# Performance work log

Hardware: AMD Instinct MI355X
Metric: run time of the kernel (lower is better)

## Reference

```python
import jax, jax.numpy as jnp
import numpy as np


def log_g(x):
    # faithful to torch: where(x>=0, log(relu(x)+0.5), 5 - softplus(-x))
    return jnp.where(x >= 0, jnp.log(jax.nn.relu(x) + 0.5), 5.0 - jax.nn.softplus(-x))


def setup_inputs() -> dict:
    key = jax.random.key(0)
    ks = jax.random.split(key, 6)
    B, T, D, H = 8, 4096, 1024, 1024
    s = 1.0 / np.sqrt(D)
    return {
        "x": jax.random.normal(ks[0], (B, T, D), jnp.float32),
        "h_0": jax.random.normal(ks[1], (B, 1, H), jnp.float32),
        "Wz_w": jax.random.normal(ks[2], (D, H), jnp.float32) * s,
        "Wz_b": jax.random.normal(ks[3], (H,), jnp.float32) * 0.1,
        "Wh_w": jax.random.normal(ks[4], (D, H), jnp.float32) * s,
        "Wh_b": jax.random.normal(ks[5], (H,), jnp.float32) * 0.1,
    }


def reference(x, h_0, Wz_w, Wz_b, Wh_w, Wh_b):
    # k = W_z(x)
    k = jnp.einsum('btd,dh->bth', x, Wz_w) + Wz_b
    log_z = -jax.nn.softplus(-k)          # log sigmoid(k)
    log_coeffs = -jax.nn.softplus(k)      # log(1 - sigmoid(k))
    log_h0 = log_g(h_0)                                            # [B,1,H]
    log_tilde_h = log_g(jnp.einsum('btd,dh->bth', x, Wh_w) + Wh_b)  # [B,T,H]
    log_values = jnp.concatenate([log_h0, log_z + log_tilde_h], axis=1)  # [B,T+1,H]
    # a_star = pad(cumsum(log_coeffs, dim=1), (0,0,1,0)) -> one zero row at t=0
    a_star = jnp.pad(jnp.cumsum(log_coeffs, axis=1), ((0, 0), (1, 0), (0, 0)))  # [B,T+1,H]
    log_h = a_star + jax.lax.cumlogsumexp(log_values - a_star, axis=1)
    return jnp.exp(log_h)[:, 1:]  # [B,T,H]
```

## Files before the change

### kernel.cpp

```cpp
#include <hip/hip_runtime.h>
#include <hip/hip_bf16.h>
#include <stdint.h>

#define B_   8
#define T_   4096
#define D_   1024
#define H_   1024
#define M_   (B_ * T_)
#define NC_  64
#define TC_  64


typedef __attribute__((ext_vector_type(4))) float f32x4;
typedef __attribute__((ext_vector_type(8))) short bfr8;
typedef _Float16 f16;
typedef __attribute__((ext_vector_type(2))) _Float16 f16x2;

__device__ __forceinline__ unsigned short f2bf(float f) {
  unsigned int u = __float_as_uint(f);
  u += 0x7fffu + ((u >> 16) & 1u);
  return (unsigned short)(u >> 16);
}
__device__ __forceinline__ float bf2f(unsigned short h) {
  return __uint_as_float(((unsigned int)h) << 16);
}

__device__ __forceinline__ void gload16(const void* g, void* l) {
  __builtin_amdgcn_global_load_lds((const __attribute__((address_space(1))) void*)g,
                                   (__attribute__((address_space(3))) void*)l,
                                   16, 0, 0);
}

__device__ __forceinline__ float g_of(float hv) {
  return (hv >= 0.f) ? (hv + 0.5f)
                     : 148.4131591025766f / (1.f + __expf(-hv));
}

__global__ void prep_w2(const float* __restrict__ Wz, const float* __restrict__ Wh,
                        unsigned short* __restrict__ wtp, float* __restrict__ whT,
                        unsigned int* __restrict__ fcnt)
{
  int kt = blockIdx.x;
  int nt = blockIdx.y;
  int m  = blockIdx.z;
  if (kt == 0 && nt == 0 && m == 0 && threadIdx.x == 0) *fcnt = 0u;
  __shared__ float tile[32][129];
  const float* W = m ? Wh : Wz;
  int n0 = nt * 128, k0 = kt * 32;
  int t = threadIdx.x;
  {
    int r = t >> 3, c0 = (t & 7) * 16;
    const float* src = &W[(size_t)(k0 + r) * 1024 + n0 + c0];
#pragma unroll
    for (int i = 0; i < 16; i++) tile[r][c0 + i] = src[i];
  }
  __syncthreads();
  unsigned short* out = wtp + ((size_t)(m * 8 + nt) * 32 + kt) * 8192;
  int n = t >> 1, hf = t & 1;
#pragma unroll
  for (int c4 = 0; c4 < 4; c4++) {
    int c = hf * 4 + c4;
    int s = c ^ (n & 7);
    unsigned int u[4];
#pragma unroll
    for (int q = 0; q < 4; q++) {
      unsigned short w2[2];
#pragma unroll
      for (int e2 = 0; e2 < 2; e2++) {
        int e = q * 2 + e2;
        float v = tile[(s & 3) * 8 + e][n];
        unsigned short hi = f2bf(v);
        w2[e2] = (s < 4) ? hi : f2bf(v - bf2f(hi));
      }
      u[q] = (unsigned int)w2[0] | ((unsigned int)w2[1] << 16);
    }
    *(uint4*)&out[(size_t)n * 64 + c * 8] = make_uint4(u[0], u[1], u[2], u[3]);
  }
  if (m == 1) {
#pragma unroll
    for (int i = 0; i < 16; i++)
      whT[(size_t)(n0 + n) * 1024 + k0 + hf * 16 + i] = tile[hf * 16 + i][n];
  }
}

__global__ __launch_bounds__(512, 2) void gemm_cv(
    const float* __restrict__ x,
    const unsigned short* __restrict__ wtp,
    const float* __restrict__ bz, const float* __restrict__ bhb,
    f16x2* __restrict__ cvbuf,
    unsigned int* __restrict__ fcnt, unsigned int* __restrict__ flist,
    unsigned int fcap)
{
  __shared__ __align__(16) unsigned short Ac[2][16384];
  __shared__ __align__(16) unsigned short Bz[2][8192];
  __shared__ __align__(16) unsigned short Bh[2][8192];
  int tid = threadIdx.x;
  int lane = tid & 63, wv = tid >> 6;
  int wm = wv >> 2, wn = wv & 3;
  int lrow = lane & 15, lq = lane >> 4;

  int bid = blockIdx.x;
  int cpx = gridDim.x >> 3;
  int swz = (bid & 7) * cpx + (bid >> 3);
  int nt = swz & 7;
  int mt = swz >> 3;
  int m0 = mt * 256, n0 = nt * 128;

  f32x4 accz[8][2], acch[8][2];
#pragma unroll
  for (int i = 0; i < 8; i++)
#pragma unroll
    for (int j = 0; j < 2; j++) {
      accz[i][j] = (f32x4){0.f, 0.f, 0.f, 0.f};
      acch[i][j] = (f32x4){0.f, 0.f, 0.f, 0.f};
    }

  int art = tid >> 1, half = tid & 1;
  int r7 = art & 7;
  int c0 = (((half * 2)     ) ^ r7) << 3;
  int c1 = (((half * 2) + 1) ^ r7) << 3;
  int abw = art * 64;
  const float* xp = x + (size_t)(m0 + art) * D_ + half * 16;

  int fch = (lq ^ (lrow & 7)) << 3;
  int abase = (wm * 128 + lrow) * 64 + fch;
  int bbase = (wn * 32 + lrow) * 64 + fch;

  const unsigned short* bsz = wtp + (size_t)nt * 262144;
  const unsigned short* bsh = bsz + 2097152;

  uint4 xa[4];

  auto loadX = [&](int kt) {
#pragma unroll
    for (int q = 0; q < 4; q++)
      xa[q] = *(const uint4*)(xp + (size_t)kt * 32 + q * 4);
  };
  auto stageB = [&](int kt, int nb) {
    size_t o = (size_t)kt * 8192 + tid * 8;
    gload16(bsz + o,        &Bz[nb][tid * 8]);
    gload16(bsz + o + 4096, &Bz[nb][4096 + tid * 8]);
    gload16(bsh + o,        &Bh[nb][tid * 8]);
    gload16(bsh + o + 4096, &Bh[nb][4096 + tid * 8]);
  };
  auto writeA = [&](int nb) {
    unsigned int h00 = __builtin_amdgcn_perm(xa[0].y, xa[0].x, 0x07060302u);
    unsigned int h01 = __builtin_amdgcn_perm(xa[0].w, xa[0].z, 0x07060302u);
    unsigned int h02 = __builtin_amdgcn_perm(xa[1].y, xa[1].x, 0x07060302u);
    unsigned int h03 = __builtin_amdgcn_perm(xa[1].w, xa[1].z, 0x07060302u);
    unsigned int h10 = __builtin_amdgcn_perm(xa[2].y, xa[2].x, 0x07060302u);
    unsigned int h11 = __builtin_amdgcn_perm(xa[2].w, xa[2].z, 0x07060302u);
    unsigned int h12 = __builtin_amdgcn_perm(xa[3].y, xa[3].x, 0x07060302u);
    unsigned int h13 = __builtin_amdgcn_perm(xa[3].w, xa[3].z, 0x07060302u);
    unsigned int l00, l01, l02, l03, l10, l11, l12, l13;
    {
      float a0 = __uint_as_float(xa[0].x) - __uint_as_float(xa[0].x & 0xffff0000u);
      float a1 = __uint_as_float(xa[0].y) - __uint_as_float(xa[0].y & 0xffff0000u);
      float a2 = __uint_as_float(xa[0].z) - __uint_as_float(xa[0].z & 0xffff0000u);
      float a3 = __uint_as_float(xa[0].w) - __uint_as_float(xa[0].w & 0xffff0000u);
      float b0 = __uint_as_float(xa[1].x) - __uint_as_float(xa[1].x & 0xffff0000u);
      float b1 = __uint_as_float(xa[1].y) - __uint_as_float(xa[1].y & 0xffff0000u);
      float b2 = __uint_as_float(xa[1].z) - __uint_as_float(xa[1].z & 0xffff0000u);
      float b3 = __uint_as_float(xa[1].w) - __uint_as_float(xa[1].w & 0xffff0000u);
      l00 = __builtin_amdgcn_perm(__float_as_uint(a1), __float_as_uint(a0), 0x07060302u);
      l01 = __builtin_amdgcn_perm(__float_as_uint(a3), __float_as_uint(a2), 0x07060302u);
      l02 = __builtin_amdgcn_perm(__float_as_uint(b1), __float_as_uint(b0), 0x07060302u);
      l03 = __builtin_amdgcn_perm(__float_as_uint(b3), __float_as_uint(b2), 0x07060302u);
    }
    {
      float a0 = __uint_as_float(xa[2].x) - __uint_as_float(xa[2].x & 0xffff0000u);
      float a1 = __uint_as_float(xa[2].y) - __uint_as_float(xa[2].y & 0xffff0000u);
      float a2 = __uint_as_float(xa[2].z) - __uint_as_float(xa[2].z & 0xffff0000u);
      float a3 = __uint_as_float(xa[2].w) - __uint_as_float(xa[2].w & 0xffff0000u);
      float b0 = __uint_as_float(xa[3].x) - __uint_as_float(xa[3].x & 0xffff0000u);
      float b1 = __uint_as_float(xa[3].y) - __uint_as_float(xa[3].y & 0xffff0000u);
      float b2 = __uint_as_float(xa[3].z) - __uint_as_float(xa[3].z & 0xffff0000u);
      float b3 = __uint_as_float(xa[3].w) - __uint_as_float(xa[3].w & 0xffff0000u);
      l10 = __builtin_amdgcn_perm(__float_as_uint(a1), __float_as_uint(a0), 0x07060302u);
      l11 = __builtin_amdgcn_perm(__float_as_uint(a3), __float_as_uint(a2), 0x07060302u);
      l12 = __builtin_amdgcn_perm(__float_as_uint(b1), __float_as_uint(b0), 0x07060302u);
      l13 = __builtin_amdgcn_perm(__float_as_uint(b3), __float_as_uint(b2), 0x07060302u);
    }
    *(uint4*)&Ac[nb][abw + c0]        = make_uint4(h00, h01, h02, h03);
    *(uint4*)&Ac[nb][abw + c1]        = make_uint4(h10, h11, h12, h13);
    *(uint4*)&Ac[nb][(abw + c0) ^ 32] = make_uint4(l00, l01, l02, l03);
    *(uint4*)&Ac[nb][(abw + c1) ^ 32] = make_uint4(l10, l11, l12, l13);
  };
  auto mfma_tile = [&](int cur) {
    bfr8 bzh[2], bzl[2], bhh[2], bhl[2];
#pragma unroll
    for (int j = 0; j < 2; j++) {
      int o = bbase + j * 1024;
      bzh[j] = *(const bfr8*)&Bz[cur][o];
      bzl[j] = *(const bfr8*)&Bz[cur][o ^ 32];
      bhh[j] = *(const bfr8*)&Bh[cur][o];
      bhl[j] = *(const bfr8*)&Bh[cur][o ^ 32];
    }
    __builtin_amdgcn_s_setprio(1);
#pragma unroll
    for (int i = 0; i < 8; i++) {
      int o = abase + i * 1024;
      bfr8 ah = *(const bfr8*)&Ac[cur][o];
      bfr8 al = *(const bfr8*)&Ac[cur][o ^ 32];
#pragma unroll
      for (int j = 0; j < 2; j++) {
        accz[i][j] = __builtin_amdgcn_mfma_f32_16x16x32_bf16(ah, bzh[j], accz[i][j], 0, 0, 0);
        accz[i][j] = __builtin_amdgcn_mfma_f32_16x16x32_bf16(al, bzh[j], accz[i][j], 0, 0, 0);
        accz[i][j] = __builtin_amdgcn_mfma_f32_16x16x32_bf16(ah, bzl[j], accz[i][j], 0, 0, 0);
        acch[i][j] = __builtin_amdgcn_mfma_f32_16x16x32_bf16(ah, bhh[j], acch[i][j], 0, 0, 0);
        acch[i][j] = __builtin_amdgcn_mfma_f32_16x16x32_bf16(al, bhh[j], acch[i][j], 0, 0, 0);
        acch[i][j] = __builtin_amdgcn_mfma_f32_16x16x32_bf16(ah, bhl[j], acch[i][j], 0, 0, 0);
      }
    }
    __builtin_amdgcn_s_setprio(0);
  };

  loadX(0);
  stageB(0, 0);
  writeA(0);
  asm volatile("s_waitcnt vmcnt(0) lgkmcnt(0)" ::: "memory");
  __builtin_amdgcn_sched_barrier(0);
  __builtin_amdgcn_s_barrier();

  auto kstep = [&](int kt, int cur) {
    loadX(kt + 1);
    stageB(kt + 1, cur ^ 1);
    mfma_tile(cur);
    writeA(cur ^ 1);
    asm volatile("s_waitcnt vmcnt(0) lgkmcnt(0)" ::: "memory");
    __builtin_amdgcn_sched_barrier(0);
    __builtin_amdgcn_s_barrier();
  };

#pragma unroll 1
  for (int kt = 0; kt < 30; kt += 2) {
    kstep(kt, 0);
    kstep(kt + 1, 1);
  }
  kstep(30, 0);
  mfma_tile(1);

#pragma unroll
  for (int j = 0; j < 2; j++) {
    int col = n0 + wn * 32 + j * 16 + lrow;
    float kb = bz[col], hb = bhb[col];
#pragma unroll
    for (int i = 0; i < 8; i++) {
      int row0 = m0 + wm * 128 + i * 16 + lq * 4;
#pragma unroll
      for (int r = 0; r < 4; r++) {
        float kv = accz[i][j][r] + kb;
        float hv = acch[i][j][r] + hb;
        f16 kf = (f16)kv;
        float c  = 1.f / (1.f + __expf((float)kf));
        float v  = (1.f - c) * g_of(hv);
        size_t off = (size_t)(row0 + r) * H_ + col;
        f16x2 pr; pr[0] = kf; pr[1] = (f16)v;
        cvbuf[off] = pr;
        if (__builtin_fabsf(hv) < 1e-3f) {
          unsigned int p = atomicAdd(fcnt, 1u);
          if (p < fcap) flist[p] = (unsigned int)off;
        }
      }
    }
  }
}

__global__ void fixup_kc512(const float* __restrict__ x, const float* __restrict__ whT,
                            const float* __restrict__ bhb, f16x2* cvbuf,
                            const unsigned int* __restrict__ fcnt,
                            const unsigned int* __restrict__ flist, unsigned int fcap)
{
  unsigned int n = *fcnt; if (n > fcap) n = fcap;
  unsigned int gtid = blockIdx.x * blockDim.x + threadIdx.x;
  unsigned int nt = gridDim.x * blockDim.x;
  const unsigned int lim = (unsigned int)M_ * (unsigned int)H_;
  for (unsigned int i = gtid; i < n; i += nt) {
    unsigned int o = flist[i];
    if (o >= lim) continue;
    unsigned int row = o >> 10, col = o & 1023u;
    const float* xr = x + (size_t)row * D_;
    const float* wr = whT + (size_t)col * D_;
    float a1 = 0.f, a2 = 0.f;
    for (int d = 0; d < 512; d++)
      a1 = fmaf(xr[d], wr[d], a1);
    for (int d = 512; d < 1024; d++)
      a2 = fmaf(xr[d], wr[d], a2);
    float hs = (a1 + a2) + bhb[col];
    float g  = (hs >= 0.f) ? (hs + 0.5f)
                           : 148.4131591025766f / (1.f + __expf(-hs));
    f16x2 pr = cvbuf[o];
    float z  = 1.f / (1.f + __expf(-(float)pr[0]));
    pr[1] = (f16)(z * g);
    cvbuf[o] = pr;
  }
}

__global__ void scan_p1(const f16x2* __restrict__ cv,
                        float* __restrict__ Cc, float* __restrict__ Vv)
{
  int h = blockIdx.x * 256 + threadIdx.x;
  int ch = blockIdx.y, b = blockIdx.z;
  size_t base = ((size_t)b * T_ + (size_t)ch * TC_) * H_ + h;
  float C = 1.f, V = 0.f;
#pragma unroll 4
  for (int i = 0; i < TC_; i++) {
    f16x2 p = cv[base + (size_t)i * H_];
    float c = 1.f / (1.f + __expf((float)p[0]));
    V = fmaf(c, V, (float)p[1]);
    C *= c;
  }
  size_t o = ((size_t)b * NC_ + ch) * H_ + h;
  Cc[o] = C; Vv[o] = V;
}

__global__ void scan_p2(const float* __restrict__ h0, const float* __restrict__ Cc,
                        const float* __restrict__ Vv, float* __restrict__ Hi)
{
  int idx = blockIdx.x * 256 + threadIdx.x;
  float hs = g_of(h0[idx]);
  int b = idx >> 10, h = idx & 1023;
  for (int ch = 0; ch < NC_; ch++) {
    size_t o = ((size_t)b * NC_ + ch) * H_ + h;
    Hi[o] = hs;
    hs = fmaf(Cc[o], hs, Vv[o]);
  }
}

__global__ void scan_p3(void* buf, const float* __restrict__ Hi)
{
  __shared__ f16x2 S[TC_][256];
  const f16x2* cv = (const f16x2*)buf;
  float* out = (float*)buf;
  int t = threadIdx.x;
  int hg = blockIdx.x, ch = blockIdx.y, b = blockIdx.z;
  int col = hg * 256 + t;
  size_t base = ((size_t)b * T_ + (size_t)ch * TC_) * H_ + col;
#pragma unroll 4
  for (int r = 0; r < TC_; r++)
    S[r][t] = cv[base + (size_t)r * H_];
  __syncthreads();
  float hs = Hi[((size_t)b * NC_ + ch) * H_ + col];
#pragma unroll 4
  for (int r = 0; r < TC_; r++) {
    f16x2 p = S[r][t];
    float c = 1.f / (1.f + __expf((float)p[0]));
    hs = fmaf(c, hs, (float)p[1]);
    out[base + (size_t)r * H_] = hs;
  }
}

extern "C" void kernel_launch(void* const* d_in, const int* in_sizes, int n_in,
                              void* d_out, int out_size, void* d_ws, size_t ws_size,
                              hipStream_t stream)
{
  const float* x  = (const float*)d_in[0];
  const float* h0 = (const float*)d_in[1];
  const float* Wz = (const float*)d_in[2];
  const float* bz = (const float*)d_in[3];
  const float* Wh = (const float*)d_in[4];
  const float* bh = (const float*)d_in[5];
  char* ws = (char*)d_ws;

  const size_t MiB = 1024u * 1024u;
  unsigned int* fcnt  = (unsigned int*)(ws);
  unsigned int* flist = (unsigned int*)(ws + 4096);
  const unsigned int fcap = 250u * 1024u;
  unsigned short* wtp = (unsigned short*)(ws + 2 * MiB);
  float* Cc = (float*)(ws + 10 * MiB);
  float* Vv = (float*)(ws + 12 * MiB);
  float* Hi = (float*)(ws + 14 * MiB);
  float* whT = (float*)(ws + 16 * MiB);

  f16x2* cvbuf = (f16x2*)d_out;

  prep_w2<<<dim3(32, 8, 2), 256, 0, stream>>>(Wz, Wh, wtp, whT, fcnt);
  gemm_cv<<<1024, 512, 0, stream>>>(x, wtp, bz, bh, cvbuf, fcnt, flist, fcap);
  fixup_kc512<<<512, 256, 0, stream>>>(x, whT, bh, cvbuf, fcnt, flist, fcap);
  scan_p1<<<dim3(4, 64, 8), 256, 0, stream>>>(cvbuf, Cc, Vv);
  scan_p2<<<32, 256, 0, stream>>>(h0, Cc, Vv, Hi);
  scan_p3<<<dim3(4, 64, 8), 256, 0, stream>>>(d_out, Hi);
}
```

Measured before the change: 747.2 us.

## Drop LDS double buffering in gemm_cv to raise occupancy

The GEMM kernel's double-buffered LDS tiles for A, Bz and Bh become single buffers, which halves LDS use per block. The launch-bounds occupancy hint goes from 2 to 4. The explicit prefetch pipeline (waitcnt, sched_barrier, s_setprio) is replaced by a simple loop: stage, __syncthreads, compute, __syncthreads. The aim is to hide latency through more resident waves instead of software pipelining. In exchange, the tighter register budget may spill the large MFMA accumulators. Global-to-LDS loads also get no overlap within a block, and a plain __syncthreads may not wait for the async LDS loads.

```diff
diff --git a/kernel.cpp b/kernel.cpp
--- a/kernel.cpp
+++ b/kernel.cpp
@@ -83,7 +83,7 @@
   }
 }
 
-__global__ __launch_bounds__(512, 2) void gemm_cv(
+__global__ __launch_bounds__(512, 4) void gemm_cv(
     const float* __restrict__ x,
     const unsigned short* __restrict__ wtp,
     const float* __restrict__ bz, const float* __restrict__ bhb,
@@ -91,9 +91,9 @@
     unsigned int* __restrict__ fcnt, unsigned int* __restrict__ flist,
     unsigned int fcap)
 {
-  __shared__ __align__(16) unsigned short Ac[2][16384];
-  __shared__ __align__(16) unsigned short Bz[2][8192];
-  __shared__ __align__(16) unsigned short Bh[2][8192];
+  __shared__ __align__(16) unsigned short Ac[16384];
+  __shared__ __align__(16) unsigned short Bz[8192];
+  __shared__ __align__(16) unsigned short Bh[8192];
   int tid = threadIdx.x;
   int lane = tid & 63, wv = tid >> 6;
   int wm = wv >> 2, wn = wv & 3;
@@ -136,14 +136,14 @@
     for (int q = 0; q < 4; q++)
       xa[q] = *(const uint4*)(xp + (size_t)kt * 32 + q * 4);
   };
-  auto stageB = [&](int kt, int nb) {
+  auto stageB = [&](int kt) {
     size_t o = (size_t)kt * 8192 + tid * 8;
-    gload16(bsz + o,        &Bz[nb][tid * 8]);
-    gload16(bsz + o + 4096, &Bz[nb][4096 + tid * 8]);
-    gload16(bsh + o,        &Bh[nb][tid * 8]);
-    gload16(bsh + o + 4096, &Bh[nb][4096 + tid * 8]);
+    gload16(bsz + o,        &Bz[tid * 8]);
+    gload16(bsz + o + 4096, &Bz[4096 + tid * 8]);
+    gload16(bsh + o,        &Bh[tid * 8]);
+    gload16(bsh + o + 4096, &Bh[4096 + tid * 8]);
   };
-  auto writeA = [&](int nb) {
+  auto writeA = [&]() {
     unsigned int h00 = __builtin_amdgcn_perm(xa[0].y, xa[0].x, 0x07060302u);
     unsigned int h01 = __builtin_amdgcn_perm(xa[0].w, xa[0].z, 0x07060302u);
     unsigned int h02 = __builtin_amdgcn_perm(xa[1].y, xa[1].x, 0x07060302u);
@@ -181,27 +181,26 @@
       l12 = __builtin_amdgcn_perm(__float_as_uint(b1), __float_as_uint(b0), 0x07060302u);
       l13 = __builtin_amdgcn_perm(__float_as_uint(b3), __float_as_uint(b2), 0x07060302u);
     }
-    *(uint4*)&Ac[nb][abw + c0]        = make_uint4(h00, h01, h02, h03);
-    *(uint4*)&Ac[nb][abw + c1]        = make_uint4(h10, h11, h12, h13);
-    *(uint4*)&Ac[nb][(abw + c0) ^ 32] = make_uint4(l00, l01, l02, l03);
-    *(uint4*)&Ac[nb][(abw + c1) ^ 32] = make_uint4(l10, l11, l12, l13);
+    *(uint4*)&Ac[abw + c0]        = make_uint4(h00, h01, h02, h03);
+    *(uint4*)&Ac[abw + c1]        = make_uint4(h10, h11, h12, h13);
+    *(uint4*)&Ac[(abw + c0) ^ 32] = make_uint4(l00, l01, l02, l03);
+    *(uint4*)&Ac[(abw + c1) ^ 32] = make_uint4(l10, l11, l12, l13);
   };
-  auto mfma_tile = [&](int cur) {
+  auto mfma_tile = [&]() {
     bfr8 bzh[2], bzl[2], bhh[2], bhl[2];
 #pragma unroll
     for (int j = 0; j < 2; j++) {
       int o = bbase + j * 1024;
-      bzh[j] = *(const bfr8*)&Bz[cur][o];
-      bzl[j] = *(const bfr8*)&Bz[cur][o ^ 32];
-      bhh[j] = *(const bfr8*)&Bh[cur][o];
-      bhl[j] = *(const bfr8*)&Bh[cur][o ^ 32];
-    }
-    __builtin_amdgcn_s_setprio(1);
+      bzh[j] = *(const bfr8*)&Bz[o];
+      bzl[j] = *(const bfr8*)&Bz[o ^ 32];
+      bhh[j] = *(const bfr8*)&Bh[o];
+      bhl[j] = *(const bfr8*)&Bh[o ^ 32];
+    }
 #pragma unroll
     for (int i = 0; i < 8; i++) {
       int o = abase + i * 1024;
-      bfr8 ah = *(const bfr8*)&Ac[cur][o];
-      bfr8 al = *(const bfr8*)&Ac[cur][o ^ 32];
+      bfr8 ah = *(const bfr8*)&Ac[o];
+      bfr8 al = *(const bfr8*)&Ac[o ^ 32];
 #pragma unroll
       for (int j = 0; j < 2; j++) {
         accz[i][j] = __builtin_amdgcn_mfma_f32_16x16x32_bf16(ah, bzh[j], accz[i][j], 0, 0, 0);
@@ -212,33 +211,18 @@
         acch[i][j] = __builtin_amdgcn_mfma_f32_16x16x32_bf16(ah, bhl[j], acch[i][j], 0, 0, 0);
       }
     }
-    __builtin_amdgcn_s_setprio(0);
   };
 
   loadX(0);
-  stageB(0, 0);
-  writeA(0);
-  asm volatile("s_waitcnt vmcnt(0) lgkmcnt(0)" ::: "memory");
-  __builtin_amdgcn_sched_barrier(0);
-  __builtin_amdgcn_s_barrier();
-
-  auto kstep = [&](int kt, int cur) {
-    loadX(kt + 1);
-    stageB(kt + 1, cur ^ 1);
-    mfma_tile(cur);
-    writeA(cur ^ 1);
-    asm volatile("s_waitcnt vmcnt(0) lgkmcnt(0)" ::: "memory");
-    __builtin_amdgcn_sched_barrier(0);
-    __builtin_amdgcn_s_barrier();
-  };
-
 #pragma unroll 1
-  for (int kt = 0; kt < 30; kt += 2) {
-    kstep(kt, 0);
-    kstep(kt + 1, 1);
-  }
-  kstep(30, 0);
-  mfma_tile(1);
+  for (int kt = 0; kt < 32; ++kt) {
+    stageB(kt);
+    writeA();
+    __syncthreads();
+    if (kt < 31) loadX(kt + 1);
+    mfma_tile();
+    if (kt < 31) __syncthreads();
+  }
 
 #pragma unroll
   for (int j = 0; j < 2; j++) {
```

Measured after the change: 2.072 ms. +177.3%, slower.
